# Kernel tuning notes

Hardware: AMD Instinct MI355X
Metric: run time of the kernel (lower is better)

The kernel has to match this reference:

```python
import jax, jax.numpy as jnp
import numpy as np

EMBED_DIM = 256
NUM_HEADS = 4
HEAD_DIM = EMBED_DIM // NUM_HEADS
SCALE = HEAD_DIM ** (-0.5)


def setup_inputs() -> dict:
    key = jax.random.key(0)
    kx, kq, kp, kb = jax.random.split(key, 4)
    B, N, C = 4, 4096, EMBED_DIM
    x = jax.random.normal(kx, (B, N, C), dtype=jnp.float32)
    # qkv: Linear(C, 3C, bias=False); torch stores weight as [out, in]
    w_qkv = jax.random.normal(kq, (3 * C, C), dtype=jnp.float32) * (C ** -0.5)
    w_proj = jax.random.normal(kp, (C, C), dtype=jnp.float32) * (C ** -0.5)
    b_proj = jax.random.normal(kb, (C,), dtype=jnp.float32) * 0.01
    return {"x": x, "w_qkv": w_qkv, "w_proj": w_proj, "b_proj": b_proj}


def reference(x, w_qkv, w_proj, b_proj):
    B, N, C = x.shape
    H, D = NUM_HEADS, HEAD_DIM
    # qkv projection: [B,N,3C] -> [3,B,H,N,D]
    qkv = (x @ w_qkv.T).reshape(B, N, 3, H, D).transpose(2, 0, 3, 1, 4)
    q, k, v = qkv[0], qkv[1], qkv[2]
    # materialized [B,H,N,N] scores (faithful to the original)
    attn = jnp.einsum("bhnd,bhmd->bhnm", q, k) * SCALE
    attn_probs = jax.nn.softmax(attn, axis=-1)
    out = jnp.einsum("bhnm,bhmd->bhnd", attn_probs, v)
    out = out.transpose(0, 2, 1, 3).reshape(B, N, C)
    return out @ w_proj.T + b_proj
```

## Files before the change

kernel.cpp:

```cpp
#include <hip/hip_runtime.h>
#include <hip/hip_bf16.h>

typedef __hip_bfloat16 bf16;
typedef _Float16 f16;
typedef __attribute__((ext_vector_type(8))) short bf16x8;
typedef __attribute__((ext_vector_type(8))) _Float16 f16x8;
typedef __attribute__((ext_vector_type(2))) _Float16 f16x2;
typedef __attribute__((ext_vector_type(4))) float f32x4;
typedef __attribute__((ext_vector_type(4))) unsigned int u32x4;
typedef __attribute__((ext_vector_type(2))) unsigned int u32x2;

#define B_ 4
#define N_ 4096
#define C_ 256
#define H_ 4
#define D_ 64
#define KLN 0.18033688011112042f

#if __has_builtin(__builtin_amdgcn_exp2f)
#define EXP2(x) __builtin_amdgcn_exp2f(x)
#else
#define EXP2(x) exp2f(x)
#endif
#if __has_builtin(__builtin_amdgcn_rcpf)
#define RCP(x) __builtin_amdgcn_rcpf(x)
#else
#define RCP(x) (1.0f / (x))
#endif

__device__ inline void load_lds16(const void* g, void* l) {
#if __has_builtin(__builtin_amdgcn_global_load_lds)
    __builtin_amdgcn_global_load_lds(
        (const __attribute__((address_space(1))) unsigned int*)g,
        (__attribute__((address_space(3))) unsigned int*)l, 16, 0, 0);
#else
    int ln = __lane_id();
    ((u32x4*)l)[ln] = *((const u32x4*)g);
#endif
}

__device__ inline unsigned int pk2(float a, float b) {
    unsigned int ua = __builtin_bit_cast(unsigned int, a) + 0x8000u;
    unsigned int ub = __builtin_bit_cast(unsigned int, b) + 0x8000u;
    return (ua >> 16) | (ub & 0xffff0000u);
}
__device__ inline unsigned int pkh2(float a, float b) {
#if __has_builtin(__builtin_amdgcn_cvt_pkrtz)
    return __builtin_bit_cast(unsigned int, __builtin_amdgcn_cvt_pkrtz(a, b));
#else
    f16x2 h = { (f16)a, (f16)b };
    return __builtin_bit_cast(unsigned int, h);
#endif
}
__device__ inline short f2s(float x) {
    return (short)__builtin_bit_cast(unsigned short, __float2bfloat16(x));
}
__device__ inline bf16x8 cvt8(const float* __restrict__ p) {
    f32x4 a = *reinterpret_cast<const f32x4*>(p);
    f32x4 b = *reinterpret_cast<const f32x4*>(p + 4);
    bf16x8 r = { f2s(a[0]), f2s(a[1]), f2s(a[2]), f2s(a[3]),
                 f2s(b[0]), f2s(b[1]), f2s(b[2]), f2s(b[3]) };
    return r;
}

__global__ __launch_bounds__(256) void cast_bf16(const float* __restrict__ x,
                                                 const float* __restrict__ wq,
                                                 const float* __restrict__ wp,
                                                 bf16* __restrict__ xb,
                                                 bf16* __restrict__ wqb,
                                                 bf16* __restrict__ wpb)
{
    int bid = blockIdx.x;
    const float* s; bf16* d; int base;
    if (bid < 2048)      { s = x;  d = xb;  base = bid * 2048; }
    else if (bid < 2144) { s = wq; d = wqb; base = (bid - 2048) * 2048; }
    else                 { s = wp; d = wpb; base = (bid - 2144) * 2048; }
    int i = base + threadIdx.x * 8;
    f32x4 a = *reinterpret_cast<const f32x4*>(s + i);
    f32x4 b = *reinterpret_cast<const f32x4*>(s + i + 4);
    u32x4 o;
    o.x = pk2(a[0], a[1]); o.y = pk2(a[2], a[3]);
    o.z = pk2(b[0], b[1]); o.w = pk2(b[2], b[3]);
    *reinterpret_cast<u32x4*>(d + i) = o;
}

__global__ __launch_bounds__(256, 2) void qkv_fast(const bf16* __restrict__ x,
                                                   const bf16* __restrict__ w,
                                                   bf16* __restrict__ qw,
                                                   bf16* __restrict__ kw,
                                                   f16* __restrict__ vtw)
{
    __shared__ short w_s[64][264];
    const int tid  = threadIdx.x;
    const int lane = tid & 63;
    const int wav  = tid >> 6;
    const int quad = lane >> 4;
    const int l16  = lane & 15;
    const int bid = (blockIdx.x & 7) * 384 + (blockIdx.x >> 3);
    const int mt = bid / 12, nb = bid % 12;
    const int m0 = mt * 64, n0 = nb * 64;

    {
        const int row = tid >> 2, cb = (tid & 3) * 64;
        const bf16* src = w + (size_t)(n0 + row) * C_ + cb;
#pragma unroll
        for (int i = 0; i < 8; ++i)
            *reinterpret_cast<bf16x8*>(&w_s[row][cb + i * 8]) =
                *reinterpret_cast<const bf16x8*>(src + i * 8);
    }
    __syncthreads();

    f32x4 acc[4] = {{0,0,0,0},{0,0,0,0},{0,0,0,0},{0,0,0,0}};
    const bf16* xrow = x + (size_t)(m0 + wav * 16 + l16) * C_ + quad * 8;
    if (nb < 8) {
#pragma unroll
        for (int k0 = 0; k0 < C_; k0 += 32) {
            bf16x8 a = *reinterpret_cast<const bf16x8*>(xrow + k0);
#pragma unroll
            for (int nt = 0; nt < 4; ++nt) {
                bf16x8 b = *reinterpret_cast<const bf16x8*>(&w_s[nt * 16 + l16][k0 + quad * 8]);
                acc[nt] = __builtin_amdgcn_mfma_f32_16x16x32_bf16(b, a, acc[nt], 0, 0, 0);
            }
        }
    } else {
#pragma unroll
        for (int k0 = 0; k0 < C_; k0 += 32) {
            bf16x8 a = *reinterpret_cast<const bf16x8*>(xrow + k0);
#pragma unroll
            for (int nt = 0; nt < 4; ++nt) {
                bf16x8 b = *reinterpret_cast<const bf16x8*>(&w_s[nt * 16 + l16][k0 + quad * 8]);
                acc[nt] = __builtin_amdgcn_mfma_f32_16x16x32_bf16(a, b, acc[nt], 0, 0, 0);
            }
        }
    }

    const int bb = m0 >> 12;
    const int nbase = (m0 + wav * 16) & (N_ - 1);
    if (nb < 4) {
        bf16* dst = qw + (((size_t)bb * H_ + nb) * N_ + nbase + l16) * D_;
#pragma unroll
        for (int nt = 0; nt < 4; ++nt) {
            u32x2 wv = { pk2(acc[nt][0] * KLN, acc[nt][1] * KLN),
                         pk2(acc[nt][2] * KLN, acc[nt][3] * KLN) };
            *reinterpret_cast<u32x2*>(dst + nt * 16 + quad * 4) = wv;
        }
    } else if (nb < 8) {
        bf16* dst = kw + (((size_t)bb * H_ + (nb - 4)) * N_ + nbase + l16) * D_;
#pragma unroll
        for (int nt = 0; nt < 4; ++nt) {
            u32x2 wv = { pk2(acc[nt][0], acc[nt][1]),
                         pk2(acc[nt][2], acc[nt][3]) };
            *reinterpret_cast<u32x2*>(dst + nt * 16 + quad * 4) = wv;
        }
    } else {
        const int h = nb - 8;
#pragma unroll
        for (int nt = 0; nt < 4; ++nt) {
            int d = nt * 16 + l16;
            u32x2 wv;
            wv.x = pkh2(acc[nt][0], acc[nt][1]);
            wv.y = pkh2(acc[nt][2], acc[nt][3]);
            *reinterpret_cast<u32x2*>(
                vtw + (((size_t)bb * H_ + h) * D_ + d) * N_ + nbase + quad * 4) = wv;
        }
    }
}

__global__ __launch_bounds__(256) void qkv_cvt(const float* __restrict__ x,
                                               const float* __restrict__ w,
                                               bf16* __restrict__ qw,
                                               bf16* __restrict__ kw,
                                               f16* __restrict__ vtw)
{
    const int lane = threadIdx.x & 63;
    const int wav  = threadIdx.x >> 6;
    const int quad = lane >> 4;
    const int l16  = lane & 15;
    const int gw   = blockIdx.x * 4 + wav;
    const int m0   = (gw / 12) * 16;
    const int n0   = (gw % 12) * 64;

    f32x4 acc[4] = {{0,0,0,0},{0,0,0,0},{0,0,0,0},{0,0,0,0}};
    const float* xrow = x + (size_t)(m0 + l16) * C_ + quad * 8;
#pragma unroll
    for (int k0 = 0; k0 < C_; k0 += 32) {
        bf16x8 a = cvt8(xrow + k0);
#pragma unroll
        for (int nt = 0; nt < 4; ++nt) {
            bf16x8 b = cvt8(w + (size_t)(n0 + nt * 16 + l16) * C_ + k0 + quad * 8);
            acc[nt] = __builtin_amdgcn_mfma_f32_16x16x32_bf16(a, b, acc[nt], 0, 0, 0);
        }
    }
#pragma unroll
    for (int nt = 0; nt < 4; ++nt)
#pragma unroll
        for (int r = 0; r < 4; ++r) {
            int m  = m0 + quad * 4 + r;
            int o  = n0 + nt * 16 + l16;
            int bb = m >> 12;
            int n  = m & (N_ - 1);
            if (o < 256) {
                int h = o >> 6, d = o & 63;
                qw[(((size_t)bb * H_ + h) * N_ + n) * D_ + d] =
                    __float2bfloat16(acc[nt][r] * KLN);
            } else if (o < 512) {
                int oo = o - 256; int h = oo >> 6, d = oo & 63;
                kw[(((size_t)bb * H_ + h) * N_ + n) * D_ + d] =
                    __float2bfloat16(acc[nt][r]);
            } else {
                int oo = o - 512; int h = oo >> 6, d = oo & 63;
                vtw[(((size_t)bb * H_ + h) * D_ + d) * N_ + n] = (f16)acc[nt][r];
            }
        }
}

__global__ __launch_bounds__(512, 4) void attn(const bf16* __restrict__ q,
                                               const bf16* __restrict__ k,
                                               const f16* __restrict__ vt,
                                               bf16* __restrict__ o)
{
    __shared__ __align__(16) char smem[65536];
    short* k_s = reinterpret_cast<short*>(smem);
    f16*   v_s = reinterpret_cast<f16*>(smem + 32768);

    const int tid  = threadIdx.x;
    const int lane = tid & 63;
    const int wav  = tid >> 6;
    const int quad = lane >> 4;
    const int l16  = lane & 15;
    const int l8   = lane & 7;
    const int sub  = wav & 3;
    const int jh   = wav >> 2;

    const int wg = (blockIdx.x & 7) * 64 + (blockIdx.x >> 3);
    const int bh = wg >> 5;
    const int qt = wg & 31;
    const int bb = bh >> 2, h = bh & 3;

    const bf16* qp = q  + (size_t)bh * N_ * D_;
    const bf16* kp = k  + (size_t)bh * N_ * D_;
    const f16*  vp = vt + (size_t)bh * D_ * N_;

    const int qbase = qt * 128 + sub * 32;
    bf16x8 qb[2][2];
#pragma unroll
    for (int qg = 0; qg < 2; ++qg)
#pragma unroll
        for (int ks = 0; ks < 2; ++ks)
            qb[qg][ks] = *reinterpret_cast<const bf16x8*>(
                qp + (size_t)(qbase + qg * 16 + l16) * D_ + ks * 32 + quad * 8);

    const int ri = lane >> 3;
    const int ci = lane & 7;
    const int gc = ci ^ ri;
    int koff[2], voff[2], lds_r[2];
#pragma unroll
    for (int g = 0; g < 2; ++g) {
        const int rb  = sub * 16 + g * 8;
        const int rho = rb + ri;
        const int pr  = (rho & 32) | ((rho & 12) << 1) | ((rho & 16) >> 2) | (rho & 3);
        koff[g]  = pr * D_ + gc * 8;
        voff[g]  = rho * N_ + gc * 8;
        lds_r[g] = rb * 64;
    }

    f32x4 oacc[2][4];
    f32x4 lacc[2];
#pragma unroll
    for (int qg = 0; qg < 2; ++qg) {
        lacc[qg] = (f32x4){0, 0, 0, 0};
#pragma unroll
        for (int dt = 0; dt < 4; ++dt) oacc[qg][dt] = (f32x4){0, 0, 0, 0};
    }
    const f16x8 onesA = {1.f16, 1.f16, 1.f16, 1.f16, 1.f16, 1.f16, 1.f16, 1.f16};

    auto stage = [&](int buf, int t) {
        const int j0 = jh * 2048 + t * 64;
        short* kd = k_s + (size_t)(buf * 2 + jh) * 4096;
        f16*   vd = v_s + (size_t)(buf * 2 + jh) * 4096;
#pragma unroll
        for (int g = 0; g < 2; ++g) {
            load_lds16(kp + (size_t)j0 * D_ + koff[g], kd + lds_r[g]);
            load_lds16(vp + j0 + voff[g],              vd + lds_r[g]);
        }
    };

    stage(0, 0);
    __syncthreads();

    for (int t = 0; t < 32; ++t) {
        const int cur = t & 1;
        if (t < 31) stage(cur ^ 1, t + 1);

        const short* kt  = k_s + (size_t)(cur * 2 + jh) * 4096;
        const f16*   vtl = v_s + (size_t)(cur * 2 + jh) * 4096;

        f32x4 s[2][4];
#pragma unroll
        for (int qg = 0; qg < 2; ++qg)
#pragma unroll
            for (int nt = 0; nt < 4; ++nt) s[qg][nt] = (f32x4){0, 0, 0, 0};
#pragma unroll
        for (int nt = 0; nt < 4; ++nt) {
            const int rb = (nt * 16 + l16) * 64;
            bf16x8 k0 = *reinterpret_cast<const bf16x8*>(kt + rb + ((quad    ) ^ l8) * 8);
            bf16x8 k1 = *reinterpret_cast<const bf16x8*>(kt + rb + ((4 + quad) ^ l8) * 8);
#pragma unroll
            for (int qg = 0; qg < 2; ++qg) {
                s[qg][nt] = __builtin_amdgcn_mfma_f32_16x16x32_bf16(k0, qb[qg][0], s[qg][nt], 0, 0, 0);
                s[qg][nt] = __builtin_amdgcn_mfma_f32_16x16x32_bf16(k1, qb[qg][1], s[qg][nt], 0, 0, 0);
            }
        }

        f16x8 pb[2][2];
#pragma unroll
        for (int qg = 0; qg < 2; ++qg)
#pragma unroll
            for (int ks = 0; ks < 2; ++ks) {
                const f32x4 sa = s[qg][2 * ks], sb = s[qg][2 * ks + 1];
                u32x4 pw;
                pw.x = pkh2(EXP2(sa[0]), EXP2(sa[1]));
                pw.y = pkh2(EXP2(sa[2]), EXP2(sa[3]));
                pw.z = pkh2(EXP2(sb[0]), EXP2(sb[1]));
                pw.w = pkh2(EXP2(sb[2]), EXP2(sb[3]));
                pb[qg][ks] = __builtin_bit_cast(f16x8, pw);
                lacc[qg] = __builtin_amdgcn_mfma_f32_16x16x32_f16(onesA, pb[qg][ks], lacc[qg], 0, 0, 0);
            }

#pragma unroll
        for (int ks = 0; ks < 2; ++ks)
#pragma unroll
            for (int dt = 0; dt < 4; ++dt) {
                f16x8 va = *reinterpret_cast<const f16x8*>(
                    vtl + (dt * 16 + l16) * 64 + (((ks << 2) + quad) ^ l8) * 8);
#pragma unroll
                for (int qg = 0; qg < 2; ++qg)
                    oacc[qg][dt] = __builtin_amdgcn_mfma_f32_16x16x32_f16(va, pb[qg][ks], oacc[qg][dt], 0, 0, 0);
            }

        __syncthreads();
    }

    float* mrg = reinterpret_cast<float*>(smem);
    const int slot = (sub * 64 + lane) * 35;
    if (jh == 1) {
#pragma unroll
        for (int qg = 0; qg < 2; ++qg) {
#pragma unroll
            for (int dt = 0; dt < 4; ++dt)
#pragma unroll
                for (int e = 0; e < 4; ++e)
                    mrg[slot + qg * 17 + dt * 4 + e] = oacc[qg][dt][e];
            mrg[slot + qg * 17 + 16] = lacc[qg][0];
        }
    }
    __syncthreads();
    if (jh == 0) {
#pragma unroll
        for (int qg = 0; qg < 2; ++qg) {
            const float rl = RCP(lacc[qg][0] + mrg[slot + qg * 17 + 16]);
            const size_t obase = ((size_t)bb * N_ + qbase + qg * 16 + l16) * C_ + h * D_;
#pragma unroll
            for (int dt = 0; dt < 4; ++dt) {
                float v0 = (oacc[qg][dt][0] + mrg[slot + qg * 17 + dt * 4 + 0]) * rl;
                float v1 = (oacc[qg][dt][1] + mrg[slot + qg * 17 + dt * 4 + 1]) * rl;
                float v2 = (oacc[qg][dt][2] + mrg[slot + qg * 17 + dt * 4 + 2]) * rl;
                float v3 = (oacc[qg][dt][3] + mrg[slot + qg * 17 + dt * 4 + 3]) * rl;
                u32x2 wv = { pk2(v0, v1), pk2(v2, v3) };
                *reinterpret_cast<u32x2*>(o + obase + dt * 16 + quad * 4) = wv;
            }
        }
    }
}

__global__ __launch_bounds__(256, 2) void out_proj_fast(const bf16* __restrict__ ov,
                                                        const bf16* __restrict__ w,
                                                        const float* __restrict__ bias,
                                                        float* __restrict__ out)
{
    __shared__ short w_s[64][264];
    const int tid  = threadIdx.x;
    const int lane = tid & 63;
    const int wav  = tid >> 6;
    const int quad = lane >> 4;
    const int l16  = lane & 15;
    const int bid = (blockIdx.x & 7) * 128 + (blockIdx.x >> 3);
    const int m0 = (bid >> 2) * 64;
    const int n0 = (bid & 3) * 64;

    {
        const int row = tid >> 2, cb = (tid & 3) * 64;
        const bf16* src = w + (size_t)(n0 + row) * C_ + cb;
#pragma unroll
        for (int i = 0; i < 8; ++i)
            *reinterpret_cast<bf16x8*>(&w_s[row][cb + i * 8]) =
                *reinterpret_cast<const bf16x8*>(src + i * 8);
    }
    __syncthreads();

    f32x4 acc[4] = {{0,0,0,0},{0,0,0,0},{0,0,0,0},{0,0,0,0}};
    const bf16* orow = ov + (size_t)(m0 + wav * 16 + l16) * C_ + quad * 8;
#pragma unroll
    for (int k0 = 0; k0 < C_; k0 += 32) {
        bf16x8 a = *reinterpret_cast<const bf16x8*>(orow + k0);
#pragma unroll
        for (int nt = 0; nt < 4; ++nt) {
            bf16x8 b = *reinterpret_cast<const bf16x8*>(&w_s[nt * 16 + l16][k0 + quad * 8]);
            acc[nt] = __builtin_amdgcn_mfma_f32_16x16x32_bf16(b, a, acc[nt], 0, 0, 0);
        }
    }
    const int m = m0 + wav * 16 + l16;
#pragma unroll
    for (int nt = 0; nt < 4; ++nt) {
        const int oc0 = n0 + nt * 16 + quad * 4;
        f32x4 bv = *reinterpret_cast<const f32x4*>(bias + oc0);
        f32x4 ovv = acc[nt] + bv;
        *reinterpret_cast<f32x4*>(out + (size_t)m * C_ + oc0) = ovv;
    }
}

__global__ __launch_bounds__(256) void out_proj_cvt(const bf16* __restrict__ ov,
                                                    const float* __restrict__ w,
                                                    const float* __restrict__ bias,
                                                    float* __restrict__ out)
{
    const int lane = threadIdx.x & 63;
    const int wav  = threadIdx.x >> 6;
    const int quad = lane >> 4;
    const int l16  = lane & 15;
    const int gw   = blockIdx.x * 4 + wav;
    const int m0   = (gw >> 2) * 16;
    const int n0   = (gw & 3) * 64;

    f32x4 acc[4] = {{0,0,0,0},{0,0,0,0},{0,0,0,0},{0,0,0,0}};
    const bf16* orow = ov + (size_t)(m0 + l16) * C_ + quad * 8;
#pragma unroll
    for (int k0 = 0; k0 < C_; k0 += 32) {
        bf16x8 a = *reinterpret_cast<const bf16x8*>(orow + k0);
#pragma unroll
        for (int nt = 0; nt < 4; ++nt) {
            bf16x8 b = cvt8(w + (size_t)(n0 + nt * 16 + l16) * C_ + k0 + quad * 8);
            acc[nt] = __builtin_amdgcn_mfma_f32_16x16x32_bf16(a, b, acc[nt], 0, 0, 0);
        }
    }
#pragma unroll
    for (int nt = 0; nt < 4; ++nt)
#pragma unroll
        for (int r = 0; r < 4; ++r) {
            int m  = m0 + quad * 4 + r;
            int oc = n0 + nt * 16 + l16;
            out[(size_t)m * C_ + oc] = acc[nt][r] + bias[oc];
        }
}

extern "C" void kernel_launch(void* const* d_in, const int* in_sizes, int n_in,
                              void* d_out, int out_size, void* d_ws, size_t ws_size,
                              hipStream_t stream) {
    const float* x      = (const float*)d_in[0];
    const float* w_qkv  = (const float*)d_in[1];
    const float* w_proj = (const float*)d_in[2];
    const float* b_proj = (const float*)d_in[3];
    float* out = (float*)d_out;

    const size_t qkv_elems = (size_t)B_ * H_ * N_ * D_;
    bf16* q_ws  = (bf16*)d_ws;
    bf16* k_ws  = q_ws  + qkv_elems;
    f16*  vt_ws = (f16*)(k_ws + qkv_elems);
    bf16* o_ws  = (bf16*)(vt_ws + qkv_elems);
    bf16* x_bf  = o_ws  + qkv_elems;
    bf16* wq_bf = x_bf  + (size_t)B_ * N_ * C_;
    bf16* wp_bf = wq_bf + (size_t)3 * C_ * C_;

    const size_t need = ((size_t)4 * qkv_elems + (size_t)B_ * N_ * C_
                         + (size_t)3 * C_ * C_ + (size_t)C_ * C_) * 2;

    if (ws_size >= need) {
        cast_bf16    <<<2176, 256, 0, stream>>>(x, w_qkv, w_proj, x_bf, wq_bf, wp_bf);
        qkv_fast     <<<3072, 256, 0, stream>>>(x_bf, wq_bf, q_ws, k_ws, vt_ws);
        attn         <<< 512, 512, 0, stream>>>(q_ws, k_ws, vt_ws, o_ws);
        out_proj_fast<<<1024, 256, 0, stream>>>(o_ws, wp_bf, b_proj, out);
    } else {
        qkv_cvt      <<<3072, 256, 0, stream>>>(x, w_qkv, q_ws, k_ws, vt_ws);
        attn         <<< 512, 512, 0, stream>>>(q_ws, k_ws, vt_ws, o_ws);
        out_proj_cvt <<<1024, 256, 0, stream>>>(o_ws, w_proj, b_proj, out);
    }
}
```

Baseline: 181.9 us.

## Double M-tile in projection GEMMs, VALU row sums and setprio in attention

The QKV and output projection kernels now process two 64-row halves per block, reusing the shared-memory weight tile and halving the grid. The attention kernel replaces the ones-vector MFMA row-sum with VALU accumulation of exp values plus a final cross-lane shuffle reduction. It also seeds the first score MFMA with a zero accumulator instead of zeroing registers, and wraps the MFMA sections in s_setprio. The trade-off is fewer blocks and less parallelism in the GEMMs, and more VALU work in the softmax loop.

```diff
diff --git a/kernel.cpp b/kernel.cpp
--- a/kernel.cpp
+++ b/kernel.cpp
@@ -96,9 +96,9 @@
     const int wav  = tid >> 6;
     const int quad = lane >> 4;
     const int l16  = lane & 15;
-    const int bid = (blockIdx.x & 7) * 384 + (blockIdx.x >> 3);
+    const int bid = (blockIdx.x & 7) * 192 + (blockIdx.x >> 3);
     const int mt = bid / 12, nb = bid % 12;
-    const int m0 = mt * 64, n0 = nb * 64;
+    const int m0 = mt * 128, n0 = nb * 64;
 
     {
         const int row = tid >> 2, cb = (tid & 3) * 64;
@@ -110,58 +110,62 @@
     }
     __syncthreads();
 
-    f32x4 acc[4] = {{0,0,0,0},{0,0,0,0},{0,0,0,0},{0,0,0,0}};
-    const bf16* xrow = x + (size_t)(m0 + wav * 16 + l16) * C_ + quad * 8;
-    if (nb < 8) {
-#pragma unroll
-        for (int k0 = 0; k0 < C_; k0 += 32) {
-            bf16x8 a = *reinterpret_cast<const bf16x8*>(xrow + k0);
+#pragma unroll
+    for (int half = 0; half < 2; ++half) {
+        const int mh = m0 + half * 64;
+        f32x4 acc[4] = {{0,0,0,0},{0,0,0,0},{0,0,0,0},{0,0,0,0}};
+        const bf16* xrow = x + (size_t)(mh + wav * 16 + l16) * C_ + quad * 8;
+        if (nb < 8) {
+#pragma unroll
+            for (int k0 = 0; k0 < C_; k0 += 32) {
+                bf16x8 a = *reinterpret_cast<const bf16x8*>(xrow + k0);
+#pragma unroll
+                for (int nt = 0; nt < 4; ++nt) {
+                    bf16x8 b = *reinterpret_cast<const bf16x8*>(&w_s[nt * 16 + l16][k0 + quad * 8]);
+                    acc[nt] = __builtin_amdgcn_mfma_f32_16x16x32_bf16(b, a, acc[nt], 0, 0, 0);
+                }
+            }
+        } else {
+#pragma unroll
+            for (int k0 = 0; k0 < C_; k0 += 32) {
+                bf16x8 a = *reinterpret_cast<const bf16x8*>(xrow + k0);
+#pragma unroll
+                for (int nt = 0; nt < 4; ++nt) {
+                    bf16x8 b = *reinterpret_cast<const bf16x8*>(&w_s[nt * 16 + l16][k0 + quad * 8]);
+                    acc[nt] = __builtin_amdgcn_mfma_f32_16x16x32_bf16(a, b, acc[nt], 0, 0, 0);
+                }
+            }
+        }
+
+        const int bb = mh >> 12;
+        const int nbase = (mh + wav * 16) & (N_ - 1);
+        if (nb < 4) {
+            bf16* dst = qw + (((size_t)bb * H_ + nb) * N_ + nbase + l16) * D_;
 #pragma unroll
             for (int nt = 0; nt < 4; ++nt) {
-                bf16x8 b = *reinterpret_cast<const bf16x8*>(&w_s[nt * 16 + l16][k0 + quad * 8]);
-                acc[nt] = __builtin_amdgcn_mfma_f32_16x16x32_bf16(b, a, acc[nt], 0, 0, 0);
-            }
-        }
-    } else {
-#pragma unroll
-        for (int k0 = 0; k0 < C_; k0 += 32) {
-            bf16x8 a = *reinterpret_cast<const bf16x8*>(xrow + k0);
+                u32x2 wv = { pk2(acc[nt][0] * KLN, acc[nt][1] * KLN),
+                             pk2(acc[nt][2] * KLN, acc[nt][3] * KLN) };
+                *reinterpret_cast<u32x2*>(dst + nt * 16 + quad * 4) = wv;
+            }
+        } else if (nb < 8) {
+            bf16* dst = kw + (((size_t)bb * H_ + (nb - 4)) * N_ + nbase + l16) * D_;
 #pragma unroll
             for (int nt = 0; nt < 4; ++nt) {
-                bf16x8 b = *reinterpret_cast<const bf16x8*>(&w_s[nt * 16 + l16][k0 + quad * 8]);
-                acc[nt] = __builtin_amdgcn_mfma_f32_16x16x32_bf16(a, b, acc[nt], 0, 0, 0);
-            }
-        }
-    }
-
-    const int bb = m0 >> 12;
-    const int nbase = (m0 + wav * 16) & (N_ - 1);
-    if (nb < 4) {
-        bf16* dst = qw + (((size_t)bb * H_ + nb) * N_ + nbase + l16) * D_;
-#pragma unroll
-        for (int nt = 0; nt < 4; ++nt) {
-            u32x2 wv = { pk2(acc[nt][0] * KLN, acc[nt][1] * KLN),
-                         pk2(acc[nt][2] * KLN, acc[nt][3] * KLN) };
-            *reinterpret_cast<u32x2*>(dst + nt * 16 + quad * 4) = wv;
-        }
-    } else if (nb < 8) {
-        bf16* dst = kw + (((size_t)bb * H_ + (nb - 4)) * N_ + nbase + l16) * D_;
-#pragma unroll
-        for (int nt = 0; nt < 4; ++nt) {
-            u32x2 wv = { pk2(acc[nt][0], acc[nt][1]),
-                         pk2(acc[nt][2], acc[nt][3]) };
-            *reinterpret_cast<u32x2*>(dst + nt * 16 + quad * 4) = wv;
-        }
-    } else {
-        const int h = nb - 8;
-#pragma unroll
-        for (int nt = 0; nt < 4; ++nt) {
-            int d = nt * 16 + l16;
-            u32x2 wv;
-            wv.x = pkh2(acc[nt][0], acc[nt][1]);
-            wv.y = pkh2(acc[nt][2], acc[nt][3]);
-            *reinterpret_cast<u32x2*>(
-                vtw + (((size_t)bb * H_ + h) * D_ + d) * N_ + nbase + quad * 4) = wv;
+                u32x2 wv = { pk2(acc[nt][0], acc[nt][1]),
+                             pk2(acc[nt][2], acc[nt][3]) };
+                *reinterpret_cast<u32x2*>(dst + nt * 16 + quad * 4) = wv;
+            }
+        } else {
+            const int h = nb - 8;
+#pragma unroll
+            for (int nt = 0; nt < 4; ++nt) {
+                int d = nt * 16 + l16;
+                u32x2 wv;
+                wv.x = pkh2(acc[nt][0], acc[nt][1]);
+                wv.y = pkh2(acc[nt][2], acc[nt][3]);
+                *reinterpret_cast<u32x2*>(
+                    vtw + (((size_t)bb * H_ + h) * D_ + d) * N_ + nbase + quad * 4) = wv;
+            }
         }
     }
 }
@@ -265,14 +269,13 @@
     }
 
     f32x4 oacc[2][4];
-    f32x4 lacc[2];
+    f32x4 lv[2];
 #pragma unroll
     for (int qg = 0; qg < 2; ++qg) {
-        lacc[qg] = (f32x4){0, 0, 0, 0};
+        lv[qg] = (f32x4){0, 0, 0, 0};
 #pragma unroll
         for (int dt = 0; dt < 4; ++dt) oacc[qg][dt] = (f32x4){0, 0, 0, 0};
     }
-    const f16x8 onesA = {1.f16, 1.f16, 1.f16, 1.f16, 1.f16, 1.f16, 1.f16, 1.f16};
 
     auto stage = [&](int buf, int t) {
         const int j0 = jh * 2048 + t * 64;
@@ -296,10 +299,7 @@
         const f16*   vtl = v_s + (size_t)(cur * 2 + jh) * 4096;
 
         f32x4 s[2][4];
-#pragma unroll
-        for (int qg = 0; qg < 2; ++qg)
-#pragma unroll
-            for (int nt = 0; nt < 4; ++nt) s[qg][nt] = (f32x4){0, 0, 0, 0};
+        __builtin_amdgcn_s_setprio(1);
 #pragma unroll
         for (int nt = 0; nt < 4; ++nt) {
             const int rb = (nt * 16 + l16) * 64;
@@ -307,10 +307,13 @@
             bf16x8 k1 = *reinterpret_cast<const bf16x8*>(kt + rb + ((4 + quad) ^ l8) * 8);
 #pragma unroll
             for (int qg = 0; qg < 2; ++qg) {
-                s[qg][nt] = __builtin_amdgcn_mfma_f32_16x16x32_bf16(k0, qb[qg][0], s[qg][nt], 0, 0, 0);
-                s[qg][nt] = __builtin_amdgcn_mfma_f32_16x16x32_bf16(k1, qb[qg][1], s[qg][nt], 0, 0, 0);
-            }
-        }
+                s[qg][nt] = __builtin_amdgcn_mfma_f32_16x16x32_bf16(
+                    k0, qb[qg][0], (f32x4){0.f, 0.f, 0.f, 0.f}, 0, 0, 0);
+                s[qg][nt] = __builtin_amdgcn_mfma_f32_16x16x32_bf16(
+                    k1, qb[qg][1], s[qg][nt], 0, 0, 0);
+            }
+        }
+        __builtin_amdgcn_s_setprio(0);
 
         f16x8 pb[2][2];
 #pragma unroll
@@ -318,15 +321,19 @@
 #pragma unroll
             for (int ks = 0; ks < 2; ++ks) {
                 const f32x4 sa = s[qg][2 * ks], sb = s[qg][2 * ks + 1];
+                f32x4 pa = { EXP2(sa[0]), EXP2(sa[1]), EXP2(sa[2]), EXP2(sa[3]) };
+                f32x4 pc = { EXP2(sb[0]), EXP2(sb[1]), EXP2(sb[2]), EXP2(sb[3]) };
                 u32x4 pw;
-                pw.x = pkh2(EXP2(sa[0]), EXP2(sa[1]));
-                pw.y = pkh2(EXP2(sa[2]), EXP2(sa[3]));
-                pw.z = pkh2(EXP2(sb[0]), EXP2(sb[1]));
-                pw.w = pkh2(EXP2(sb[2]), EXP2(sb[3]));
+                pw.x = pkh2(pa[0], pa[1]);
+                pw.y = pkh2(pa[2], pa[3]);
+                pw.z = pkh2(pc[0], pc[1]);
+                pw.w = pkh2(pc[2], pc[3]);
                 pb[qg][ks] = __builtin_bit_cast(f16x8, pw);
-                lacc[qg] = __builtin_amdgcn_mfma_f32_16x16x32_f16(onesA, pb[qg][ks], lacc[qg], 0, 0, 0);
-            }
-
+                lv[qg] += pa;
+                lv[qg] += pc;
+            }
+
+        __builtin_amdgcn_s_setprio(1);
 #pragma unroll
         for (int ks = 0; ks < 2; ++ks)
 #pragma unroll
@@ -337,8 +344,18 @@
                 for (int qg = 0; qg < 2; ++qg)
                     oacc[qg][dt] = __builtin_amdgcn_mfma_f32_16x16x32_f16(va, pb[qg][ks], oacc[qg][dt], 0, 0, 0);
             }
+        __builtin_amdgcn_s_setprio(0);
 
         __syncthreads();
+    }
+
+    float lr[2];
+#pragma unroll
+    for (int qg = 0; qg < 2; ++qg) {
+        float l = (lv[qg][0] + lv[qg][1]) + (lv[qg][2] + lv[qg][3]);
+        l += __shfl_xor(l, 16);
+        l += __shfl_xor(l, 32);
+        lr[qg] = l;
     }
 
     float* mrg = reinterpret_cast<float*>(smem);
@@ -351,14 +368,14 @@
 #pragma unroll
                 for (int e = 0; e < 4; ++e)
                     mrg[slot + qg * 17 + dt * 4 + e] = oacc[qg][dt][e];
-            mrg[slot + qg * 17 + 16] = lacc[qg][0];
+            mrg[slot + qg * 17 + 16] = lr[qg];
         }
     }
     __syncthreads();
     if (jh == 0) {
 #pragma unroll
         for (int qg = 0; qg < 2; ++qg) {
-            const float rl = RCP(lacc[qg][0] + mrg[slot + qg * 17 + 16]);
+            const float rl = RCP(lr[qg] + mrg[slot + qg * 17 + 16]);
             const size_t obase = ((size_t)bb * N_ + qbase + qg * 16 + l16) * C_ + h * D_;
 #pragma unroll
             for (int dt = 0; dt < 4; ++dt) {
@@ -384,8 +401,8 @@
     const int wav  = tid >> 6;
     const int quad = lane >> 4;
     const int l16  = lane & 15;
-    const int bid = (blockIdx.x & 7) * 128 + (blockIdx.x >> 3);
-    const int m0 = (bid >> 2) * 64;
+    const int bid = (blockIdx.x & 7) * 64 + (blockIdx.x >> 3);
+    const int m0 = (bid >> 2) * 128;
     const int n0 = (bid & 3) * 64;
 
     {
@@ -398,24 +415,28 @@
     }
     __syncthreads();
 
-    f32x4 acc[4] = {{0,0,0,0},{0,0,0,0},{0,0,0,0},{0,0,0,0}};
-    const bf16* orow = ov + (size_t)(m0 + wav * 16 + l16) * C_ + quad * 8;
-#pragma unroll
-    for (int k0 = 0; k0 < C_; k0 += 32) {
-        bf16x8 a = *reinterpret_cast<const bf16x8*>(orow + k0);
+#pragma unroll
+    for (int half = 0; half < 2; ++half) {
+        const int mh = m0 + half * 64;
+        f32x4 acc[4] = {{0,0,0,0},{0,0,0,0},{0,0,0,0},{0,0,0,0}};
+        const bf16* orow = ov + (size_t)(mh + wav * 16 + l16) * C_ + quad * 8;
+#pragma unroll
+        for (int k0 = 0; k0 < C_; k0 += 32) {
+            bf16x8 a = *reinterpret_cast<const bf16x8*>(orow + k0);
+#pragma unroll
+            for (int nt = 0; nt < 4; ++nt) {
+                bf16x8 b = *reinterpret_cast<const bf16x8*>(&w_s[nt * 16 + l16][k0 + quad * 8]);
+                acc[nt] = __builtin_amdgcn_mfma_f32_16x16x32_bf16(b, a, acc[nt], 0, 0, 0);
+            }
+        }
+        const int m = mh + wav * 16 + l16;
 #pragma unroll
         for (int nt = 0; nt < 4; ++nt) {
-            bf16x8 b = *reinterpret_cast<const bf16x8*>(&w_s[nt * 16 + l16][k0 + quad * 8]);
-            acc[nt] = __builtin_amdgcn_mfma_f32_16x16x32_bf16(b, a, acc[nt], 0, 0, 0);
-        }
-    }
-    const int m = m0 + wav * 16 + l16;
-#pragma unroll
-    for (int nt = 0; nt < 4; ++nt) {
-        const int oc0 = n0 + nt * 16 + quad * 4;
-        f32x4 bv = *reinterpret_cast<const f32x4*>(bias + oc0);
-        f32x4 ovv = acc[nt] + bv;
-        *reinterpret_cast<f32x4*>(out + (size_t)m * C_ + oc0) = ovv;
+            const int oc0 = n0 + nt * 16 + quad * 4;
+            f32x4 bv = *reinterpret_cast<const f32x4*>(bias + oc0);
+            f32x4 ovv = acc[nt] + bv;
+            *reinterpret_cast<f32x4*>(out + (size_t)m * C_ + oc0) = ovv;
+        }
     }
 }
 
@@ -476,9 +497,9 @@
 
     if (ws_size >= need) {
         cast_bf16    <<<2176, 256, 0, stream>>>(x, w_qkv, w_proj, x_bf, wq_bf, wp_bf);
-        qkv_fast     <<<3072, 256, 0, stream>>>(x_bf, wq_bf, q_ws, k_ws, vt_ws);
+        qkv_fast     <<<1536, 256, 0, stream>>>(x_bf, wq_bf, q_ws, k_ws, vt_ws);
         attn         <<< 512, 512, 0, stream>>>(q_ws, k_ws, vt_ws, o_ws);
-        out_proj_fast<<<1024, 256, 0, stream>>>(o_ws, wp_bf, b_proj, out);
+        out_proj_fast<<< 512, 256, 0, stream>>>(o_ws, wp_bf, b_proj, out);
     } else {
         qkv_cvt      <<<3072, 256, 0, stream>>>(x, w_qkv, q_ws, k_ws, vt_ws);
         attn         <<< 512, 512, 0, stream>>>(q_ws, k_ws, vt_ws, o_ws);
```

Result: faster. 174.9 us (-3.9%).

## Double row tiles in projection GEMMs and serialize attention query groups

Applied to the files above, without the earlier changes.

The QKV and output projection kernels now handle 128 rows per block in two halves, reusing the shared-memory weight tile and halving the grid size. The attention inner loop loads the K fragments once, then processes the two query groups one after the other instead of interleaving them, which lowers the number of live score registers. The fallback conversion kernels and the workspace-size check are removed, and an extra barrier is added before the merge step. The intent is to amortize weight staging and to ease register pressure in attention, at the cost of fewer blocks and a weaker MFMA/exp overlap inside each wave.

```diff
diff --git a/kernel.cpp b/kernel.cpp
--- a/kernel.cpp
+++ b/kernel.cpp
@@ -51,16 +51,6 @@
     f16x2 h = { (f16)a, (f16)b };
     return __builtin_bit_cast(unsigned int, h);
 #endif
-}
-__device__ inline short f2s(float x) {
-    return (short)__builtin_bit_cast(unsigned short, __float2bfloat16(x));
-}
-__device__ inline bf16x8 cvt8(const float* __restrict__ p) {
-    f32x4 a = *reinterpret_cast<const f32x4*>(p);
-    f32x4 b = *reinterpret_cast<const f32x4*>(p + 4);
-    bf16x8 r = { f2s(a[0]), f2s(a[1]), f2s(a[2]), f2s(a[3]),
-                 f2s(b[0]), f2s(b[1]), f2s(b[2]), f2s(b[3]) };
-    return r;
 }
 
 __global__ __launch_bounds__(256) void cast_bf16(const float* __restrict__ x,
@@ -96,9 +86,9 @@
     const int wav  = tid >> 6;
     const int quad = lane >> 4;
     const int l16  = lane & 15;
-    const int bid = (blockIdx.x & 7) * 384 + (blockIdx.x >> 3);
+    const int bid = (blockIdx.x & 7) * 192 + (blockIdx.x >> 3);
     const int mt = bid / 12, nb = bid % 12;
-    const int m0 = mt * 64, n0 = nb * 64;
+    const int m0 = mt * 128, n0 = nb * 64;
 
     {
         const int row = tid >> 2, cb = (tid & 3) * 64;
@@ -110,108 +100,64 @@
     }
     __syncthreads();
 
-    f32x4 acc[4] = {{0,0,0,0},{0,0,0,0},{0,0,0,0},{0,0,0,0}};
-    const bf16* xrow = x + (size_t)(m0 + wav * 16 + l16) * C_ + quad * 8;
-    if (nb < 8) {
-#pragma unroll
-        for (int k0 = 0; k0 < C_; k0 += 32) {
-            bf16x8 a = *reinterpret_cast<const bf16x8*>(xrow + k0);
+#pragma unroll
+    for (int half = 0; half < 2; ++half) {
+        const int mh = m0 + half * 64;
+        f32x4 acc[4] = {{0,0,0,0},{0,0,0,0},{0,0,0,0},{0,0,0,0}};
+        const bf16* xrow = x + (size_t)(mh + wav * 16 + l16) * C_ + quad * 8;
+        if (nb < 8) {
+#pragma unroll
+            for (int k0 = 0; k0 < C_; k0 += 32) {
+                bf16x8 a = *reinterpret_cast<const bf16x8*>(xrow + k0);
+#pragma unroll
+                for (int nt = 0; nt < 4; ++nt) {
+                    bf16x8 b = *reinterpret_cast<const bf16x8*>(&w_s[nt * 16 + l16][k0 + quad * 8]);
+                    acc[nt] = __builtin_amdgcn_mfma_f32_16x16x32_bf16(b, a, acc[nt], 0, 0, 0);
+                }
+            }
+        } else {
+#pragma unroll
+            for (int k0 = 0; k0 < C_; k0 += 32) {
+                bf16x8 a = *reinterpret_cast<const bf16x8*>(xrow + k0);
+#pragma unroll
+                for (int nt = 0; nt < 4; ++nt) {
+                    bf16x8 b = *reinterpret_cast<const bf16x8*>(&w_s[nt * 16 + l16][k0 + quad * 8]);
+                    acc[nt] = __builtin_amdgcn_mfma_f32_16x16x32_bf16(a, b, acc[nt], 0, 0, 0);
+                }
+            }
+        }
+
+        const int bb = mh >> 12;
+        const int nbase = (mh + wav * 16) & (N_ - 1);
+        if (nb < 4) {
+            bf16* dst = qw + (((size_t)bb * H_ + nb) * N_ + nbase + l16) * D_;
 #pragma unroll
             for (int nt = 0; nt < 4; ++nt) {
-                bf16x8 b = *reinterpret_cast<const bf16x8*>(&w_s[nt * 16 + l16][k0 + quad * 8]);
-                acc[nt] = __builtin_amdgcn_mfma_f32_16x16x32_bf16(b, a, acc[nt], 0, 0, 0);
-            }
-        }
-    } else {
-#pragma unroll
-        for (int k0 = 0; k0 < C_; k0 += 32) {
-            bf16x8 a = *reinterpret_cast<const bf16x8*>(xrow + k0);
+                u32x2 wv = { pk2(acc[nt][0] * KLN, acc[nt][1] * KLN),
+                             pk2(acc[nt][2] * KLN, acc[nt][3] * KLN) };
+                *reinterpret_cast<u32x2*>(dst + nt * 16 + quad * 4) = wv;
+            }
+        } else if (nb < 8) {
+            bf16* dst = kw + (((size_t)bb * H_ + (nb - 4)) * N_ + nbase + l16) * D_;
 #pragma unroll
             for (int nt = 0; nt < 4; ++nt) {
-                bf16x8 b = *reinterpret_cast<const bf16x8*>(&w_s[nt * 16 + l16][k0 + quad * 8]);
-                acc[nt] = __builtin_amdgcn_mfma_f32_16x16x32_bf16(a, b, acc[nt], 0, 0, 0);
-            }
-        }
-    }
-
-    const int bb = m0 >> 12;
-    const int nbase = (m0 + wav * 16) & (N_ - 1);
-    if (nb < 4) {
-        bf16* dst = qw + (((size_t)bb * H_ + nb) * N_ + nbase + l16) * D_;
-#pragma unroll
-        for (int nt = 0; nt < 4; ++nt) {
-            u32x2 wv = { pk2(acc[nt][0] * KLN, acc[nt][1] * KLN),
-                         pk2(acc[nt][2] * KLN, acc[nt][3] * KLN) };
-            *reinterpret_cast<u32x2*>(dst + nt * 16 + quad * 4) = wv;
-        }
-    } else if (nb < 8) {
-        bf16* dst = kw + (((size_t)bb * H_ + (nb - 4)) * N_ + nbase + l16) * D_;
-#pragma unroll
-        for (int nt = 0; nt < 4; ++nt) {
-            u32x2 wv = { pk2(acc[nt][0], acc[nt][1]),
-                         pk2(acc[nt][2], acc[nt][3]) };
-            *reinterpret_cast<u32x2*>(dst + nt * 16 + quad * 4) = wv;
-        }
-    } else {
-        const int h = nb - 8;
-#pragma unroll
-        for (int nt = 0; nt < 4; ++nt) {
-            int d = nt * 16 + l16;
-            u32x2 wv;
-            wv.x = pkh2(acc[nt][0], acc[nt][1]);
-            wv.y = pkh2(acc[nt][2], acc[nt][3]);
-            *reinterpret_cast<u32x2*>(
-                vtw + (((size_t)bb * H_ + h) * D_ + d) * N_ + nbase + quad * 4) = wv;
-        }
-    }
-}
-
-__global__ __launch_bounds__(256) void qkv_cvt(const float* __restrict__ x,
-                                               const float* __restrict__ w,
-                                               bf16* __restrict__ qw,
-                                               bf16* __restrict__ kw,
-                                               f16* __restrict__ vtw)
-{
-    const int lane = threadIdx.x & 63;
-    const int wav  = threadIdx.x >> 6;
-    const int quad = lane >> 4;
-    const int l16  = lane & 15;
-    const int gw   = blockIdx.x * 4 + wav;
-    const int m0   = (gw / 12) * 16;
-    const int n0   = (gw % 12) * 64;
-
-    f32x4 acc[4] = {{0,0,0,0},{0,0,0,0},{0,0,0,0},{0,0,0,0}};
-    const float* xrow = x + (size_t)(m0 + l16) * C_ + quad * 8;
-#pragma unroll
-    for (int k0 = 0; k0 < C_; k0 += 32) {
-        bf16x8 a = cvt8(xrow + k0);
-#pragma unroll
-        for (int nt = 0; nt < 4; ++nt) {
-            bf16x8 b = cvt8(w + (size_t)(n0 + nt * 16 + l16) * C_ + k0 + quad * 8);
-            acc[nt] = __builtin_amdgcn_mfma_f32_16x16x32_bf16(a, b, acc[nt], 0, 0, 0);
-        }
-    }
-#pragma unroll
-    for (int nt = 0; nt < 4; ++nt)
-#pragma unroll
-        for (int r = 0; r < 4; ++r) {
-            int m  = m0 + quad * 4 + r;
-            int o  = n0 + nt * 16 + l16;
-            int bb = m >> 12;
-            int n  = m & (N_ - 1);
-            if (o < 256) {
-                int h = o >> 6, d = o & 63;
-                qw[(((size_t)bb * H_ + h) * N_ + n) * D_ + d] =
-                    __float2bfloat16(acc[nt][r] * KLN);
-            } else if (o < 512) {
-                int oo = o - 256; int h = oo >> 6, d = oo & 63;
-                kw[(((size_t)bb * H_ + h) * N_ + n) * D_ + d] =
-                    __float2bfloat16(acc[nt][r]);
-            } else {
-                int oo = o - 512; int h = oo >> 6, d = oo & 63;
-                vtw[(((size_t)bb * H_ + h) * D_ + d) * N_ + n] = (f16)acc[nt][r];
-            }
-        }
+                u32x2 wv = { pk2(acc[nt][0], acc[nt][1]),
+                             pk2(acc[nt][2], acc[nt][3]) };
+                *reinterpret_cast<u32x2*>(dst + nt * 16 + quad * 4) = wv;
+            }
+        } else {
+            const int h = nb - 8;
+#pragma unroll
+            for (int nt = 0; nt < 4; ++nt) {
+                int d = nt * 16 + l16;
+                u32x2 wv;
+                wv.x = pkh2(acc[nt][0], acc[nt][1]);
+                wv.y = pkh2(acc[nt][2], acc[nt][3]);
+                *reinterpret_cast<u32x2*>(
+                    vtw + (((size_t)bb * H_ + h) * D_ + d) * N_ + nbase + quad * 4) = wv;
+            }
+        }
+    }
 }
 
 __global__ __launch_bounds__(512, 4) void attn(const bf16* __restrict__ q,
@@ -295,52 +241,74 @@
         const short* kt  = k_s + (size_t)(cur * 2 + jh) * 4096;
         const f16*   vtl = v_s + (size_t)(cur * 2 + jh) * 4096;
 
-        f32x4 s[2][4];
-#pragma unroll
-        for (int qg = 0; qg < 2; ++qg)
-#pragma unroll
-            for (int nt = 0; nt < 4; ++nt) s[qg][nt] = (f32x4){0, 0, 0, 0};
+        bf16x8 ka[4][2];
 #pragma unroll
         for (int nt = 0; nt < 4; ++nt) {
             const int rb = (nt * 16 + l16) * 64;
-            bf16x8 k0 = *reinterpret_cast<const bf16x8*>(kt + rb + ((quad    ) ^ l8) * 8);
-            bf16x8 k1 = *reinterpret_cast<const bf16x8*>(kt + rb + ((4 + quad) ^ l8) * 8);
-#pragma unroll
-            for (int qg = 0; qg < 2; ++qg) {
-                s[qg][nt] = __builtin_amdgcn_mfma_f32_16x16x32_bf16(k0, qb[qg][0], s[qg][nt], 0, 0, 0);
-                s[qg][nt] = __builtin_amdgcn_mfma_f32_16x16x32_bf16(k1, qb[qg][1], s[qg][nt], 0, 0, 0);
-            }
-        }
-
-        f16x8 pb[2][2];
-#pragma unroll
-        for (int qg = 0; qg < 2; ++qg)
-#pragma unroll
-            for (int ks = 0; ks < 2; ++ks) {
-                const f32x4 sa = s[qg][2 * ks], sb = s[qg][2 * ks + 1];
-                u32x4 pw;
-                pw.x = pkh2(EXP2(sa[0]), EXP2(sa[1]));
-                pw.y = pkh2(EXP2(sa[2]), EXP2(sa[3]));
-                pw.z = pkh2(EXP2(sb[0]), EXP2(sb[1]));
-                pw.w = pkh2(EXP2(sb[2]), EXP2(sb[3]));
-                pb[qg][ks] = __builtin_bit_cast(f16x8, pw);
-                lacc[qg] = __builtin_amdgcn_mfma_f32_16x16x32_f16(onesA, pb[qg][ks], lacc[qg], 0, 0, 0);
-            }
-
+            ka[nt][0] = *reinterpret_cast<const bf16x8*>(kt + rb + ((quad    ) ^ l8) * 8);
+            ka[nt][1] = *reinterpret_cast<const bf16x8*>(kt + rb + ((4 + quad) ^ l8) * 8);
+        }
+
+        f32x4 s[4];
+        f16x8 pb0[2], pb1[2];
+
+#pragma unroll
+        for (int nt = 0; nt < 4; ++nt) {
+            s[nt] = __builtin_amdgcn_mfma_f32_16x16x32_bf16(
+                ka[nt][0], qb[0][0], (f32x4){0.f, 0.f, 0.f, 0.f}, 0, 0, 0);
+            s[nt] = __builtin_amdgcn_mfma_f32_16x16x32_bf16(
+                ka[nt][1], qb[0][1], s[nt], 0, 0, 0);
+        }
+#pragma unroll
+        for (int ks = 0; ks < 2; ++ks) {
+            const f32x4 sa = s[2 * ks], sb = s[2 * ks + 1];
+            u32x4 pw;
+            pw.x = pkh2(EXP2(sa[0]), EXP2(sa[1]));
+            pw.y = pkh2(EXP2(sa[2]), EXP2(sa[3]));
+            pw.z = pkh2(EXP2(sb[0]), EXP2(sb[1]));
+            pw.w = pkh2(EXP2(sb[2]), EXP2(sb[3]));
+            pb0[ks] = __builtin_bit_cast(f16x8, pw);
+            lacc[0] = __builtin_amdgcn_mfma_f32_16x16x32_f16(onesA, pb0[ks], lacc[0], 0, 0, 0);
+        }
+#pragma unroll
+        for (int nt = 0; nt < 4; ++nt) {
+            s[nt] = __builtin_amdgcn_mfma_f32_16x16x32_bf16(
+                ka[nt][0], qb[1][0], (f32x4){0.f, 0.f, 0.f, 0.f}, 0, 0, 0);
+            s[nt] = __builtin_amdgcn_mfma_f32_16x16x32_bf16(
+                ka[nt][1], qb[1][1], s[nt], 0, 0, 0);
+        }
 #pragma unroll
         for (int ks = 0; ks < 2; ++ks)
 #pragma unroll
             for (int dt = 0; dt < 4; ++dt) {
                 f16x8 va = *reinterpret_cast<const f16x8*>(
                     vtl + (dt * 16 + l16) * 64 + (((ks << 2) + quad) ^ l8) * 8);
-#pragma unroll
-                for (int qg = 0; qg < 2; ++qg)
-                    oacc[qg][dt] = __builtin_amdgcn_mfma_f32_16x16x32_f16(va, pb[qg][ks], oacc[qg][dt], 0, 0, 0);
+                oacc[0][dt] = __builtin_amdgcn_mfma_f32_16x16x32_f16(va, pb0[ks], oacc[0][dt], 0, 0, 0);
+            }
+#pragma unroll
+        for (int ks = 0; ks < 2; ++ks) {
+            const f32x4 sa = s[2 * ks], sb = s[2 * ks + 1];
+            u32x4 pw;
+            pw.x = pkh2(EXP2(sa[0]), EXP2(sa[1]));
+            pw.y = pkh2(EXP2(sa[2]), EXP2(sa[3]));
+            pw.z = pkh2(EXP2(sb[0]), EXP2(sb[1]));
+            pw.w = pkh2(EXP2(sb[2]), EXP2(sb[3]));
+            pb1[ks] = __builtin_bit_cast(f16x8, pw);
+            lacc[1] = __builtin_amdgcn_mfma_f32_16x16x32_f16(onesA, pb1[ks], lacc[1], 0, 0, 0);
+        }
+#pragma unroll
+        for (int ks = 0; ks < 2; ++ks)
+#pragma unroll
+            for (int dt = 0; dt < 4; ++dt) {
+                f16x8 va = *reinterpret_cast<const f16x8*>(
+                    vtl + (dt * 16 + l16) * 64 + (((ks << 2) + quad) ^ l8) * 8);
+                oacc[1][dt] = __builtin_amdgcn_mfma_f32_16x16x32_f16(va, pb1[ks], oacc[1][dt], 0, 0, 0);
             }
 
         __syncthreads();
     }
 
+    __syncthreads();
     float* mrg = reinterpret_cast<float*>(smem);
     const int slot = (sub * 64 + lane) * 35;
     if (jh == 1) {
@@ -384,8 +352,8 @@
     const int wav  = tid >> 6;
     const int quad = lane >> 4;
     const int l16  = lane & 15;
-    const int bid = (blockIdx.x & 7) * 128 + (blockIdx.x >> 3);
-    const int m0 = (bid >> 2) * 64;
+    const int bid = (blockIdx.x & 7) * 64 + (blockIdx.x >> 3);
+    const int m0 = (bid >> 2) * 128;
     const int n0 = (bid & 3) * 64;
 
     {
@@ -398,59 +366,29 @@
     }
     __syncthreads();
 
-    f32x4 acc[4] = {{0,0,0,0},{0,0,0,0},{0,0,0,0},{0,0,0,0}};
-    const bf16* orow = ov + (size_t)(m0 + wav * 16 + l16) * C_ + quad * 8;
-#pragma unroll
-    for (int k0 = 0; k0 < C_; k0 += 32) {
-        bf16x8 a = *reinterpret_cast<const bf16x8*>(orow + k0);
+#pragma unroll
+    for (int half = 0; half < 2; ++half) {
+        const int mh = m0 + half * 64;
+        f32x4 acc[4] = {{0,0,0,0},{0,0,0,0},{0,0,0,0},{0,0,0,0}};
+        const bf16* orow = ov + (size_t)(mh + wav * 16 + l16) * C_ + quad * 8;
+#pragma unroll
+        for (int k0 = 0; k0 < C_; k0 += 32) {
+            bf16x8 a = *reinterpret_cast<const bf16x8*>(orow + k0);
+#pragma unroll
+            for (int nt = 0; nt < 4; ++nt) {
+                bf16x8 b = *reinterpret_cast<const bf16x8*>(&w_s[nt * 16 + l16][k0 + quad * 8]);
+                acc[nt] = __builtin_amdgcn_mfma_f32_16x16x32_bf16(b, a, acc[nt], 0, 0, 0);
+            }
+        }
+        const int m = mh + wav * 16 + l16;
 #pragma unroll
         for (int nt = 0; nt < 4; ++nt) {
-            bf16x8 b = *reinterpret_cast<const bf16x8*>(&w_s[nt * 16 + l16][k0 + quad * 8]);
-            acc[nt] = __builtin_amdgcn_mfma_f32_16x16x32_bf16(b, a, acc[nt], 0, 0, 0);
-        }
-    }
-    const int m = m0 + wav * 16 + l16;
-#pragma unroll
-    for (int nt = 0; nt < 4; ++nt) {
-        const int oc0 = n0 + nt * 16 + quad * 4;
-        f32x4 bv = *reinterpret_cast<const f32x4*>(bias + oc0);
-        f32x4 ovv = acc[nt] + bv;
-        *reinterpret_cast<f32x4*>(out + (size_t)m * C_ + oc0) = ovv;
-    }
-}
-
-__global__ __launch_bounds__(256) void out_proj_cvt(const bf16* __restrict__ ov,
-                                                    const float* __restrict__ w,
-                                                    const float* __restrict__ bias,
-                                                    float* __restrict__ out)
-{
-    const int lane = threadIdx.x & 63;
-    const int wav  = threadIdx.x >> 6;
-    const int quad = lane >> 4;
-    const int l16  = lane & 15;
-    const int gw   = blockIdx.x * 4 + wav;
-    const int m0   = (gw >> 2) * 16;
-    const int n0   = (gw & 3) * 64;
-
-    f32x4 acc[4] = {{0,0,0,0},{0,0,0,0},{0,0,0,0},{0,0,0,0}};
-    const bf16* orow = ov + (size_t)(m0 + l16) * C_ + quad * 8;
-#pragma unroll
-    for (int k0 = 0; k0 < C_; k0 += 32) {
-        bf16x8 a = *reinterpret_cast<const bf16x8*>(orow + k0);
-#pragma unroll
-        for (int nt = 0; nt < 4; ++nt) {
-            bf16x8 b = cvt8(w + (size_t)(n0 + nt * 16 + l16) * C_ + k0 + quad * 8);
-            acc[nt] = __builtin_amdgcn_mfma_f32_16x16x32_bf16(a, b, acc[nt], 0, 0, 0);
-        }
-    }
-#pragma unroll
-    for (int nt = 0; nt < 4; ++nt)
-#pragma unroll
-        for (int r = 0; r < 4; ++r) {
-            int m  = m0 + quad * 4 + r;
-            int oc = n0 + nt * 16 + l16;
-            out[(size_t)m * C_ + oc] = acc[nt][r] + bias[oc];
-        }
+            const int oc0 = n0 + nt * 16 + quad * 4;
+            f32x4 bv = *reinterpret_cast<const f32x4*>(bias + oc0);
+            f32x4 ovv = acc[nt] + bv;
+            *reinterpret_cast<f32x4*>(out + (size_t)m * C_ + oc0) = ovv;
+        }
+    }
 }
 
 extern "C" void kernel_launch(void* const* d_in, const int* in_sizes, int n_in,
@@ -471,17 +409,8 @@
     bf16* wq_bf = x_bf  + (size_t)B_ * N_ * C_;
     bf16* wp_bf = wq_bf + (size_t)3 * C_ * C_;
 
-    const size_t need = ((size_t)4 * qkv_elems + (size_t)B_ * N_ * C_
-                         + (size_t)3 * C_ * C_ + (size_t)C_ * C_) * 2;
-
-    if (ws_size >= need) {
-        cast_bf16    <<<2176, 256, 0, stream>>>(x, w_qkv, w_proj, x_bf, wq_bf, wp_bf);
-        qkv_fast     <<<3072, 256, 0, stream>>>(x_bf, wq_bf, q_ws, k_ws, vt_ws);
-        attn         <<< 512, 512, 0, stream>>>(q_ws, k_ws, vt_ws, o_ws);
-        out_proj_fast<<<1024, 256, 0, stream>>>(o_ws, wp_bf, b_proj, out);
-    } else {
-        qkv_cvt      <<<3072, 256, 0, stream>>>(x, w_qkv, q_ws, k_ws, vt_ws);
-        attn         <<< 512, 512, 0, stream>>>(q_ws, k_ws, vt_ws, o_ws);
-        out_proj_cvt <<<1024, 256, 0, stream>>>(o_ws, w_proj, b_proj, out);
-    }
-}
+    cast_bf16    <<<2176, 256, 0, stream>>>(x, w_qkv, w_proj, x_bf, wq_bf, wp_bf);
+    qkv_fast     <<<1536, 256, 0, stream>>>(x_bf, wq_bf, q_ws, k_ws, vt_ws);
+    attn         <<< 512, 512, 0, stream>>>(q_ws, k_ws, vt_ws, o_ws);
+    out_proj_fast<<< 512, 256, 0, stream>>>(o_ws, wp_bf, b_proj, out);
+}
```

Result: faster. 173.0 us (median of 2 runs) (-4.9%).
